# Optimization experiments

Measured on AMD Instinct MI355X. Metric: run time of the kernel, lower is better.

Reference implementation:

```python
import jax, jax.numpy as jnp
import numpy as np


def setup_inputs() -> dict:
    key = jax.random.key(0)
    ks = jax.random.split(key, 8)
    B, L, D = 4, 2048, 2048
    H, Dh, S = 24, 64, 64
    Di = H * Dh              # 1536
    P = H * (1 + 2 * S)      # 3096
    return {
        "hidden_states": jax.random.normal(ks[0], (B, L, D), jnp.float32),
        "norm_w": jnp.ones((D,), jnp.float32),
        "in_proj_w": jax.random.normal(ks[1], (2 * Di, D), jnp.float32) * 0.02,
        "in_proj_b": jnp.zeros((2 * Di,), jnp.float32),
        "conv_w": jax.random.normal(ks[2], (Di, 1, 4), jnp.float32) * 0.2,
        "conv_b": jnp.zeros((Di,), jnp.float32),
        "x_proj_w": jax.random.normal(ks[3], (P, Di), jnp.float32) * 0.02,
        "x_proj_b": jnp.zeros((P,), jnp.float32),
        "A_log": jnp.full((H,), np.log(0.5), jnp.float32),
        "log2_alpha_base": jnp.full((H,), -1.0, jnp.float32),
        "log2_beta": jnp.zeros((H,), jnp.float32),
        "surprise_ema": jnp.ones((H,), jnp.float32),
        "out_proj_w": jax.random.normal(ks[4], (D, Di), jnp.float32) * 0.02,
        "out_proj_b": jnp.zeros((D,), jnp.float32),
        "res_gate": jnp.full((1,), 1.0 / np.sqrt(2 * 24), jnp.float32),
    }


def reference(hidden_states, norm_w, in_proj_w, in_proj_b, conv_w, conv_b,
              x_proj_w, x_proj_b, A_log, log2_alpha_base, log2_beta,
              surprise_ema, out_proj_w, out_proj_b, res_gate):
    Bsz, L, D = hidden_states.shape
    H = A_log.shape[0]
    S = (x_proj_b.shape[0] // H - 1) // 2
    Di = in_proj_w.shape[0] // 2
    Dh = Di // H
    eps = jnp.finfo(jnp.float32).eps

    # RMSNorm
    x = hidden_states * jax.lax.rsqrt(jnp.mean(hidden_states ** 2, -1, keepdims=True) + eps) * norm_w
    # in_proj -> split x/z
    xz = x @ in_proj_w.T + in_proj_b
    x, z = xz[..., :Di], xz[..., Di:]
    # causal depthwise conv1d (kernel 4, left pad 3 == torch pad=3 then [:, :L])
    xc = jax.lax.conv_general_dilated(
        x.transpose(0, 2, 1), conv_w, (1,), [(3, 0)],
        dimension_numbers=("NCH", "OIH", "NCH"), feature_group_count=Di)
    x = jax.nn.silu((xc + conv_b[None, :, None]).transpose(0, 2, 1))
    # x_proj -> dt, B, C
    xp = (x @ x_proj_w.T + x_proj_b).reshape(Bsz, L, H, 1 + 2 * S)
    dt = xp[..., 0]
    Bs = xp[..., 1:1 + S]
    Cs = xp[..., 1 + S:]
    Bs = Bs / jnp.maximum(jnp.linalg.norm(Bs, axis=-1, keepdims=True), 1e-12)
    Cs = Cs / jnp.maximum(jnp.linalg.norm(Cs, axis=-1, keepdims=True), 1e-12)
    # dt-scaled log decay (dt_scale = softplus(dt))
    A = jnp.clip(A_log, -2.3, -0.01)[None, None, :] * jax.nn.softplus(dt)
    A_decay = jnp.exp(A)                       # [B, L, H]
    X = x.reshape(Bsz, L, H, Dh)

    # surprise-gate constants (eval mode: EMA buffer fixed)
    alpha_base = 1.0 - 2.0 ** jnp.clip(log2_alpha_base, -3.32, -0.015)   # [H]
    beta = 2.0 ** jnp.clip(log2_beta, -2.0, 2.0)                          # [H]

    def step(carry, xs):
        h, h_red = carry                      # [B,H,S,Dh], [B,H,S]
        x_t, a_t, B_t, C_t = xs               # [B,H,Dh], [B,H], [B,H,S], [B,H,S]
        u_red = B_t * x_t.mean(-1)[..., None]                 # mean over Dh of outer product
        diff = (1.0 - a_t)[..., None] * u_red                 # h_new_reduced - h_expected
        pe = jnp.mean(diff ** 2, -1)                          # [B,H]
        ns = pe / (surprise_ema[None, :] + 1e-6)
        boost = jax.nn.relu(jnp.tanh(beta[None, :] * ns))
        alpha = jnp.clip(alpha_base[None, :] + (1.0 - alpha_base[None, :]) * boost, 0.01, 0.999)
        u_t = B_t[..., None] * x_t[:, :, None, :]             # [B,H,S,Dh]
        h = alpha[..., None, None] * h + (1.0 - alpha)[..., None, None] * u_t
        h_red = h.mean(-1)
        y = jnp.einsum("bhs,bhsd->bhd", C_t, h)
        return (h, h_red), y

    h0 = jnp.zeros((Bsz, H, S, Dh), jnp.float32)
    hr0 = jnp.zeros((Bsz, H, S), jnp.float32)
    xs = (X.transpose(1, 0, 2, 3), A_decay.transpose(1, 0, 2),
          Bs.transpose(1, 0, 2, 3), Cs.transpose(1, 0, 2, 3))
    _, Yt = jax.lax.scan(step, (h0, hr0), xs)                 # [L,B,H,Dh]
    Y = Yt.transpose(1, 0, 2, 3).reshape(Bsz, L, Di)
    Y = Y * jax.nn.silu(z)
    out = Y @ out_proj_w.T + out_proj_b
    return hidden_states + res_gate * out
```

## Files before the change

### kernel.cpp

```cpp
#include <hip/hip_runtime.h>
#include <stdint.h>

#define BB 4
#define LLEN 2048
#define DMODEL 2048
#define NH 24
#define DH 64
#define SS 64
#define DI 1536
#define N2 3072
#define NP 3096
#define NP_PAD 3200
#define MROWS 8192
#define NCHUNK 16
#define QC 128
#define XP2LD 136

using bf16x8 = __bf16 __attribute__((ext_vector_type(8)));
using f32x4  = float __attribute__((ext_vector_type(4)));

__device__ __forceinline__ unsigned short f2bf(float f) {
  union { float f; unsigned int u; } v; v.f = f;
  unsigned int u = v.u + 0x7fffu + ((v.u >> 16) & 1u);
  return (unsigned short)(u >> 16);
}
__device__ __forceinline__ float bf2f(unsigned short h) {
  union { unsigned int u; float f; } v; v.u = ((unsigned int)h) << 16;
  return v.f;
}

__device__ __forceinline__ void gload16(const void* g, void* l) {
  __builtin_amdgcn_global_load_lds(
    reinterpret_cast<const __attribute__((address_space(1))) void*>(reinterpret_cast<uintptr_t>(g)),
    reinterpret_cast<__attribute__((address_space(3))) void*>((uint32_t)(reinterpret_cast<uintptr_t>(l))),
    16, 0, 0);
}

__global__ __launch_bounds__(256) void k_w2bf3(
    const float* __restrict__ s0, unsigned short* __restrict__ d0, int n0,
    const float* __restrict__ s1, unsigned short* __restrict__ d1, int n1s, int n1d,
    const float* __restrict__ s2, unsigned short* __restrict__ d2, int n2) {
  int i = blockIdx.x * 256 + threadIdx.x;
  if (i < n0) { d0[i] = f2bf(s0[i]); return; }
  i -= n0;
  if (i < n1d) { d1[i] = (i < n1s) ? f2bf(s1[i]) : (unsigned short)0; return; }
  i -= n1d;
  if (i < n2) d2[i] = f2bf(s2[i]);
}

__global__ __launch_bounds__(256) void k_rmsnorm(const float* __restrict__ hs,
                                                 const float* __restrict__ w,
                                                 unsigned short* __restrict__ out) {
  const int row = blockIdx.x;
  const int t = threadIdx.x;
  const float* x = hs + (size_t)row * DMODEL;
  float4 v0 = reinterpret_cast<const float4*>(x)[t * 2 + 0];
  float4 v1 = reinterpret_cast<const float4*>(x)[t * 2 + 1];
  float ss = v0.x * v0.x + v0.y * v0.y + v0.z * v0.z + v0.w * v0.w +
             v1.x * v1.x + v1.y * v1.y + v1.z * v1.z + v1.w * v1.w;
#pragma unroll
  for (int o = 32; o; o >>= 1) ss += __shfl_xor(ss, o);
  __shared__ float red[4];
  if ((t & 63) == 0) red[t >> 6] = ss;
  __syncthreads();
  ss = red[0] + red[1] + red[2] + red[3];
  const float r = rsqrtf(ss * (1.0f / DMODEL) + 1.1920928955078125e-07f);
  float4 w0 = reinterpret_cast<const float4*>(w)[t * 2 + 0];
  float4 w1 = reinterpret_cast<const float4*>(w)[t * 2 + 1];
  union { unsigned short u[8]; uint4 v; } pk;
  pk.u[0] = f2bf(v0.x * r * w0.x); pk.u[1] = f2bf(v0.y * r * w0.y);
  pk.u[2] = f2bf(v0.z * r * w0.z); pk.u[3] = f2bf(v0.w * r * w0.w);
  pk.u[4] = f2bf(v1.x * r * w1.x); pk.u[5] = f2bf(v1.y * r * w1.y);
  pk.u[6] = f2bf(v1.z * r * w1.z); pk.u[7] = f2bf(v1.w * r * w1.w);
  *reinterpret_cast<uint4*>(out + (size_t)row * DMODEL + t * 8) = pk.v;
}

template <int EPI>
__global__ __launch_bounds__(512, 2)
void k_gemm6(const unsigned short* __restrict__ A, const unsigned short* __restrict__ B,
             const float* __restrict__ bias, void* __restrict__ Cv,
             const float* __restrict__ resid, const float* __restrict__ gatep,
             int K, int NT_N, int Nout, int ldc) {
  constexpr int AELEM = 128 * 64;
  constexpr int BUFE = AELEM + 16384;
  __shared__ alignas(16) unsigned short sm[3 * BUFE];
  const int tid = threadIdx.x;
  const int lane = tid & 63, wid = tid >> 6;
  const int wm = wid >> 2, wn = wid & 3;
  const int fr = lane & 15, kg = lane >> 4;
  const int nwg = gridDim.x;
  const int wg = ((int)blockIdx.x & 7) * (nwg >> 3) + ((int)blockIdx.x >> 3);
  const int m0 = (wg / NT_N) * 128, n0 = (wg % NT_N) * 256;
  const int NT = K >> 6;

  const unsigned short* asrc[2];
  const unsigned short* bsrc[4];
#pragma unroll
  for (int li = 0; li < 2; ++li) {
    const int gi = li * 512 + tid, r = gi >> 3, q = gi & 7;
    asrc[li] = A + (size_t)(m0 + r) * K + ((q ^ (r & 7)) << 3);
  }
#pragma unroll
  for (int li = 0; li < 4; ++li) {
    const int gi = li * 512 + tid, r = gi >> 3, q = gi & 7;
    bsrc[li] = B + (size_t)(n0 + r) * K + ((q ^ (r & 7)) << 3);
  }
  const int wlds = wid * 64;

#define STG6(buf, ko)                                                          \
  { unsigned short* da_ = sm + (buf) * BUFE;                                   \
    gload16(asrc[0] + (ko), da_ + ((0 * 512 + wlds) << 3));                    \
    gload16(asrc[1] + (ko), da_ + ((1 * 512 + wlds) << 3));                    \
    unsigned short* db_ = sm + (buf) * BUFE + AELEM;                           \
    _Pragma("unroll") for (int li = 0; li < 4; ++li)                           \
      gload16(bsrc[li] + (ko), db_ + ((li * 512 + wlds) << 3)); }

#define ARD6(bufp, f, kk)                                                      \
  (*(const bf16x8*)((bufp) + (wm * 64 + (f) * 16 + fr) * 64 +                  \
      ((((kk) * 4 + kg) ^ (fr & 7)) << 3)))
#define BRD6(bufp, nf, kk)                                                     \
  (*(const bf16x8*)((bufp) + AELEM + (wn * 64 + (nf) * 16 + fr) * 64 +         \
      ((((kk) * 4 + kg) ^ (fr & 7)) << 3)))

  f32x4 acc[4][4] = {};

  STG6(0, 0)
  STG6(1, 64)
  asm volatile("s_waitcnt vmcnt(6)" ::: "memory");
  __builtin_amdgcn_s_barrier();

  int bc_i = 0;
  for (int t = 0; t < NT; ++t) {
    unsigned short* bc = sm + bc_i * BUFE;
    const int bn_i = (bc_i + 2 >= 3) ? (bc_i - 1) : (bc_i + 2);
    const bool st = (t + 2) < NT;
    if (st) STG6(bn_i, (t + 2) << 6)

    bf16x8 bfv[4][2], af[4][2];
#pragma unroll
    for (int nf = 0; nf < 4; ++nf) {
      bfv[nf][0] = BRD6(bc, nf, 0);
      bfv[nf][1] = BRD6(bc, nf, 1);
    }
#pragma unroll
    for (int mf = 0; mf < 4; ++mf) {
      af[mf][0] = ARD6(bc, mf, 0);
      af[mf][1] = ARD6(bc, mf, 1);
    }
    __builtin_amdgcn_sched_barrier(0);
    asm volatile("s_waitcnt lgkmcnt(0)" ::: "memory");
    __builtin_amdgcn_sched_barrier(0);
    __builtin_amdgcn_s_setprio(1);
#pragma unroll
    for (int mf = 0; mf < 4; ++mf)
#pragma unroll
      for (int nf = 0; nf < 4; ++nf)
#pragma unroll
        for (int kk = 0; kk < 2; ++kk)
          acc[mf][nf] = __builtin_amdgcn_mfma_f32_16x16x32_bf16(
              af[mf][kk], bfv[nf][kk], acc[mf][nf], 0, 0, 0);
    __builtin_amdgcn_s_setprio(0);

    if (st) { asm volatile("s_waitcnt vmcnt(6)" ::: "memory"); }
    else    { asm volatile("s_waitcnt vmcnt(0)" ::: "memory"); }
    __builtin_amdgcn_s_barrier();
    bc_i = (bc_i + 1 >= 3) ? 0 : (bc_i + 1);
  }

  float* Cf = (float*)Cv;
  unsigned short* Ch = (unsigned short*)Cv;
  const float rg = (EPI == 2) ? gatep[0] : 0.f;
#pragma unroll
  for (int nf = 0; nf < 4; ++nf) {
    const int col = n0 + wn * 64 + nf * 16 + fr;
    if (col >= Nout) continue;
    const float bv = bias[col];
    int h = 0, ep = 0;
    if (EPI == 3) {
      h = col / 129;
      const int e = col - h * 129;
      ep = (e == 0) ? 128 : (e - 1);
    }
#pragma unroll
    for (int mf = 0; mf < 4; ++mf) {
      const int rowb = m0 + wm * 64 + mf * 16 + kg * 4;
#pragma unroll
      for (int r = 0; r < 4; ++r) {
        const int row = rowb + r;
        float v = acc[mf][nf][r] + bv;
        if (EPI == 3) {
          const size_t dst =
              (((size_t)((row >> 11) * NH + h) << 11) + (row & (LLEN - 1))) * XP2LD + ep;
          Ch[dst] = f2bf(v);
        } else {
          const size_t o = (size_t)row * ldc + col;
          if (EPI == 1) {
            Ch[o] = f2bf(v);
          } else {
            v = resid[o] + rg * v;
            Cf[o] = v;
          }
        }
      }
    }
  }
#undef STG6
#undef ARD6
#undef BRD6
}

__global__ __launch_bounds__(256) void k_dwconv(const unsigned short* __restrict__ xz,
                                                const float* __restrict__ cw,
                                                const float* __restrict__ cb,
                                                unsigned short* __restrict__ out) {
  const int idx = blockIdx.x * 256 + threadIdx.x;
  const int c0 = (idx % 192) * 8;
  const int bl0 = (idx / 192) * 4;
  const int lpos0 = bl0 & (LLEN - 1);
  float w[8][4];
#pragma unroll
  for (int j = 0; j < 8; ++j) {
    const float4 wv = *(const float4*)(cw + (c0 + j) * 4);
    w[j][0] = wv.x; w[j][1] = wv.y; w[j][2] = wv.z; w[j][3] = wv.w;
  }
  float xr[7][8];
#pragma unroll
  for (int m = 0; m < 7; ++m) {
    uint4 xv = make_uint4(0u, 0u, 0u, 0u);
    if (lpos0 - 3 + m >= 0)
      xv = *(const uint4*)(xz + (size_t)(bl0 - 3 + m) * N2 + c0);
    const unsigned short* xs = (const unsigned short*)&xv;
#pragma unroll
    for (int j = 0; j < 8; ++j) xr[m][j] = bf2f(xs[j]);
  }
  const float4 cb0 = *(const float4*)(cb + c0);
  const float4 cb1 = *(const float4*)(cb + c0 + 4);
  const float cbv[8] = {cb0.x, cb0.y, cb0.z, cb0.w, cb1.x, cb1.y, cb1.z, cb1.w};
#pragma unroll
  for (int t4 = 0; t4 < 4; ++t4) {
    union { unsigned short u[8]; uint4 v; } pk;
#pragma unroll
    for (int j = 0; j < 8; ++j) {
      float a = cbv[j];
#pragma unroll
      for (int k = 0; k < 4; ++k) a = fmaf(w[j][k], xr[t4 + k][j], a);
      a = a / (1.f + __expf(-a));
      pk.u[j] = f2bf(a);
    }
    *(uint4*)(out + (size_t)(bl0 + t4) * DI + c0) = pk.v;
  }
}

__global__ __launch_bounds__(256) void k_prep2(const unsigned short* __restrict__ xp2,
                                               const unsigned short* __restrict__ xc,
                                               const float* __restrict__ A_log,
                                               const float* __restrict__ l2ab,
                                               const float* __restrict__ l2b,
                                               const float* __restrict__ se,
                                               float* __restrict__ al) {
  const int blk = blockIdx.x;
  const int w = threadIdx.x >> 6, lane = threadIdx.x & 63;
  const int bl = blk / 6, hq = blk % 6;
  const int h = hq * 4 + w;
  const float xv = bf2f(xc[(size_t)bl * DI + h * DH + lane]);
  float sx = xv;
#pragma unroll
  for (int o = 32; o; o >>= 1) sx += __shfl_xor(sx, o);
  if (lane == 0) {
    const int b = bl >> 11, l = bl & (LLEN - 1);
    const size_t r2 = ((size_t)(b * NH + h) << 11) + l;
    const float xmean = sx * (1.f / 64.f);
    const float dt = bf2f(xp2[r2 * XP2LD + 128]);
    const float sp = (dt > 20.f) ? dt : log1pf(expf(dt));
    const float Ac = fminf(fmaxf(A_log[h], -2.3f), -0.01f);
    const float aa = expf(Ac * sp);
    const float one_a = 1.f - aa;
    const float pe = one_a * one_a * xmean * xmean * (1.f / 64.f);
    const float ns = pe / (se[h] + 1e-6f);
    const float beta = exp2f(fminf(fmaxf(l2b[h], -2.f), 2.f));
    const float boost = fmaxf(tanhf(beta * ns), 0.f);
    const float ab = 1.f - exp2f(fminf(fmaxf(l2ab[h], -3.32f), -0.015f));
    al[r2] = fminf(fmaxf(ab + (1.f - ab) * boost, 0.01f), 0.999f);
  }
}

__global__ __launch_bounds__(256) void k_chunk1(
    const unsigned short* __restrict__ xp2, const unsigned short* __restrict__ xcg,
    const float* __restrict__ al, unsigned short* __restrict__ xz,
    unsigned short* __restrict__ Hbuf, float* __restrict__ Dc) {
  const int blk = blockIdx.x;
  const int bh = blk >> 4, c = blk & 15;
  const int b = bh / NH, h = bh % NH;
  const int tid = threadIdx.x, w = tid >> 6, lane = tid & 63;
  const int fr = lane & 15, kg = lane >> 4;
  const int rbase = b * LLEN + c * QC;
  const size_t rbase2 = ((size_t)bh << 11) + c * QC;

  __shared__ float lc[QC], ia[QC], escl[QC], rbA[QC], rcC[QC];
  __shared__ float wtot[2];
  __shared__ alignas(16) unsigned short XT[64][152];
  __shared__ alignas(16) unsigned short BsT[64][152];
  __shared__ alignas(16) unsigned short Pt[128][88];

  float a = 1.f, la = 0.f;
  if (tid < QC) { a = al[(size_t)bh * LLEN + c * QC + tid]; la = __logf(a); }
  float s = la;
#pragma unroll
  for (int o = 1; o < 64; o <<= 1) { float t2 = __shfl_up(s, o); if (lane >= o) s += t2; }
  if (tid < QC && lane == 63) wtot[w] = s;
  __syncthreads();
  if (tid < QC) { lc[tid] = s + ((w == 1) ? wtot[0] : 0.f); ia[tid] = 1.f - a; }
  __syncthreads();
  const float lcE = lc[QC - 1];
  if (tid < QC) escl[tid] = __expf(lcE - lc[tid]);
  if (tid == 0) Dc[blk] = __expf(lcE);
  __syncthreads();

  {
    const int r8 = tid >> 3, q8 = tid & 7;
#pragma unroll
    for (int it = 0; it < 4; ++it) {
      const int u = it * 32 + r8;
      const uint4 xv = *(const uint4*)(xcg + (size_t)(rbase + u) * DI + h * DH + q8 * 8);
      const unsigned short* xs = (const unsigned short*)&xv;
#pragma unroll
      for (int j = 0; j < 8; ++j) XT[q8 * 8 + j][u] = xs[j];
      const size_t prow = (rbase2 + u) * XP2LD;
      const uint4 bv = *(const uint4*)(xp2 + prow + q8 * 8);
      const uint4 cv = *(const uint4*)(xp2 + prow + 64 + q8 * 8);
      const unsigned short* bsv = (const unsigned short*)&bv;
      const unsigned short* csv = (const unsigned short*)&cv;
      float bb[8], sb = 0.f, sc2 = 0.f;
#pragma unroll
      for (int j = 0; j < 8; ++j) {
        bb[j] = bf2f(bsv[j]);
        sb = fmaf(bb[j], bb[j], sb);
        const float cc = bf2f(csv[j]);
        sc2 = fmaf(cc, cc, sc2);
      }
      sb += __shfl_xor(sb, 1); sb += __shfl_xor(sb, 2); sb += __shfl_xor(sb, 4);
      sc2 += __shfl_xor(sc2, 1); sc2 += __shfl_xor(sc2, 2); sc2 += __shfl_xor(sc2, 4);
      const float rcpB = 1.f / fmaxf(sqrtf(sb), 1e-12f);
      const float e = escl[u] * ia[u] * rcpB;
#pragma unroll
      for (int j = 0; j < 8; ++j) BsT[q8 * 8 + j][u] = f2bf(bb[j] * e);
      if (q8 == 0) {
        rbA[u] = ia[u] * rcpB;
        rcC[u] = 1.f / fmaxf(sqrtf(sc2), 1e-12f);
      }
    }
  }
  __syncthreads();

  bf16x8 cf[2][2];
#pragma unroll
  for (int fi = 0; fi < 2; ++fi)
#pragma unroll
    for (int kk = 0; kk < 2; ++kk) {
      const int t = w * 32 + fi * 16 + fr;
      const uint4 v = *(const uint4*)(xp2 + (rbase2 + t) * XP2LD + 64 + kk * 32 + kg * 8);
      cf[fi][kk] = *(const bf16x8*)&v;
    }

  float lct[2][4], rct[2][4];
#pragma unroll
  for (int fi = 0; fi < 2; ++fi)
#pragma unroll
    for (int r = 0; r < 4; ++r) {
      const int t = w * 32 + fi * 16 + kg * 4 + r;
      lct[fi][r] = lc[t];
      rct[fi][r] = rcC[t];
    }

  f32x4 yacc[2][4] = {};
  f32x4 hacc[4] = {};
#pragma unroll
  for (int ut = 0; ut < 2; ++ut) {
    f32x4 g[2][4] = {};
#pragma unroll
    for (int kk = 0; kk < 2; ++kk)
#pragma unroll
      for (int fj = 0; fj < 4; ++fj) {
        const int u = ut * 64 + fj * 16 + fr;
        const uint4 v = *(const uint4*)(xp2 + (rbase2 + u) * XP2LD + kk * 32 + kg * 8);
        const bf16x8 bfrag = *(const bf16x8*)&v;
#pragma unroll
        for (int fi = 0; fi < 2; ++fi)
          g[fi][fj] = __builtin_amdgcn_mfma_f32_16x16x32_bf16(cf[fi][kk], bfrag, g[fi][fj], 0, 0, 0);
      }
#pragma unroll
    for (int fi = 0; fi < 2; ++fi)
#pragma unroll
      for (int fj = 0; fj < 4; ++fj) {
        const int u = ut * 64 + fj * 16 + fr;
        const float lcu = lc[u], sbu = rbA[u];
#pragma unroll
        for (int r = 0; r < 4; ++r) {
          const int t = w * 32 + fi * 16 + kg * 4 + r;
          const float v = (t >= u) ? g[fi][fj][r] * __expf(lct[fi][r] - lcu) * sbu * rct[fi][r] : 0.f;
          Pt[t][fj * 16 + fr] = f2bf(v);
        }
      }
#pragma unroll
    for (int kk = 0; kk < 2; ++kk) {
      bf16x8 xf[4];
#pragma unroll
      for (int fj = 0; fj < 4; ++fj)
        xf[fj] = *(const bf16x8*)&XT[fj * 16 + fr][ut * 64 + kk * 32 + kg * 8];
      bf16x8 pf[2];
#pragma unroll
      for (int fi = 0; fi < 2; ++fi)
        pf[fi] = *(const bf16x8*)&Pt[w * 32 + fi * 16 + fr][kk * 32 + kg * 8];
#pragma unroll
      for (int fi = 0; fi < 2; ++fi)
#pragma unroll
        for (int fj = 0; fj < 4; ++fj)
          yacc[fi][fj] = __builtin_amdgcn_mfma_f32_16x16x32_bf16(pf[fi], xf[fj], yacc[fi][fj], 0, 0, 0);
      const bf16x8 xh = *(const bf16x8*)&XT[w * 16 + fr][ut * 64 + kk * 32 + kg * 8];
#pragma unroll
      for (int fi = 0; fi < 4; ++fi) {
        const bf16x8 bs = *(const bf16x8*)&BsT[fi * 16 + fr][ut * 64 + kk * 32 + kg * 8];
        hacc[fi] = __builtin_amdgcn_mfma_f32_16x16x32_bf16(bs, xh, hacc[fi], 0, 0, 0);
      }
    }
  }
#pragma unroll
  for (int fi = 0; fi < 2; ++fi)
#pragma unroll
    for (int fj = 0; fj < 4; ++fj)
#pragma unroll
      for (int r = 0; r < 4; ++r) {
        const int t = w * 32 + fi * 16 + kg * 4 + r;
        const int d = fj * 16 + fr;
        xz[(size_t)(rbase + t) * N2 + h * DH + d] = f2bf(yacc[fi][fj][r]);
      }
  const int dcol = w * 16 + fr;
#pragma unroll
  for (int fi = 0; fi < 4; ++fi) {
    ushort4 pk;
    pk.x = f2bf(hacc[fi][0]); pk.y = f2bf(hacc[fi][1]);
    pk.z = f2bf(hacc[fi][2]); pk.w = f2bf(hacc[fi][3]);
    *(ushort4*)(Hbuf + ((size_t)blk * 64 + dcol) * 64 + fi * 16 + kg * 4) = pk;
  }
}

__global__ __launch_bounds__(256) void k_carry(unsigned short* __restrict__ Hbuf,
                                               const float* __restrict__ Dc) {
  const int bh = blockIdx.x, tid = threadIdx.x;
  float carry[16];
#pragma unroll
  for (int j = 0; j < 16; ++j) carry[j] = 0.f;
  for (int c = 0; c < NCHUNK; ++c) {
    unsigned short* p = Hbuf + (((size_t)(bh * NCHUNK + c)) << 12) + tid * 16;
    const uint4 v0 = *(const uint4*)(p);
    const uint4 v1 = *(const uint4*)(p + 8);
    const unsigned short* hs0 = (const unsigned short*)&v0;
    const unsigned short* hs1 = (const unsigned short*)&v1;
    float hl[16];
#pragma unroll
    for (int j = 0; j < 8; ++j) { hl[j] = bf2f(hs0[j]); hl[8 + j] = bf2f(hs1[j]); }
    uint4 o0, o1;
    unsigned short* os0 = (unsigned short*)&o0;
    unsigned short* os1 = (unsigned short*)&o1;
#pragma unroll
    for (int j = 0; j < 8; ++j) { os0[j] = f2bf(carry[j]); os1[j] = f2bf(carry[8 + j]); }
    *(uint4*)(p) = o0;
    *(uint4*)(p + 8) = o1;
    const float dc = Dc[bh * NCHUNK + c];
#pragma unroll
    for (int j = 0; j < 16; ++j) carry[j] = fmaf(dc, carry[j], hl[j]);
  }
}

__global__ __launch_bounds__(256) void k_chunk2(
    const unsigned short* __restrict__ xp2, const float* __restrict__ al,
    const unsigned short* __restrict__ Hbuf, const unsigned short* __restrict__ xz,
    unsigned short* __restrict__ xcg) {
  const int blk = blockIdx.x;
  const int bh = blk >> 4, c = blk & 15;
  const int b = bh / NH, h = bh % NH;
  const int tid = threadIdx.x, w = tid >> 6, lane = tid & 63;
  const int fr = lane & 15, kg = lane >> 4;
  const int rbase = b * LLEN + c * QC;
  const size_t rbase2 = ((size_t)bh << 11) + c * QC;
  __shared__ float lc[QC], rc2[QC];
  __shared__ float wtot[2];
  float a = 1.f, la = 0.f;
  if (tid < QC) { a = al[(size_t)bh * LLEN + c * QC + tid]; la = __logf(a); }
  float s = la;
#pragma unroll
  for (int o = 1; o < 64; o <<= 1) { float t2 = __shfl_up(s, o); if (lane >= o) s += t2; }
  if (tid < QC && lane == 63) wtot[w] = s;
  __syncthreads();
  if (tid < QC) lc[tid] = s + ((w == 1) ? wtot[0] : 0.f);
  __syncthreads();
  bf16x8 cf[2][2];
#pragma unroll
  for (int fi = 0; fi < 2; ++fi) {
    const int t = w * 32 + fi * 16 + fr;
    float ss = 0.f;
#pragma unroll
    for (int kk = 0; kk < 2; ++kk) {
      const uint4 v = *(const uint4*)(xp2 + (rbase2 + t) * XP2LD + 64 + kk * 32 + kg * 8);
      cf[fi][kk] = *(const bf16x8*)&v;
      const unsigned short* cs = (const unsigned short*)&v;
#pragma unroll
      for (int q = 0; q < 8; ++q) { const float cc = bf2f(cs[q]); ss = fmaf(cc, cc, ss); }
    }
    ss += __shfl_xor(ss, 16);
    ss += __shfl_xor(ss, 32);
    if (kg == 0) rc2[t] = 1.f / fmaxf(sqrtf(ss), 1e-12f);
  }
  bf16x8 hf[4][2];
#pragma unroll
  for (int fj = 0; fj < 4; ++fj)
#pragma unroll
    for (int kk = 0; kk < 2; ++kk) {
      const uint4 v = *(const uint4*)(Hbuf + ((size_t)blk * 64 + fj * 16 + fr) * 64 + kk * 32 + kg * 8);
      hf[fj][kk] = *(const bf16x8*)&v;
    }
  __syncthreads();
  f32x4 y[2][4] = {};
#pragma unroll
  for (int kk = 0; kk < 2; ++kk)
#pragma unroll
    for (int fi = 0; fi < 2; ++fi)
#pragma unroll
      for (int fj = 0; fj < 4; ++fj)
        y[fi][fj] = __builtin_amdgcn_mfma_f32_16x16x32_bf16(cf[fi][kk], hf[fj][kk], y[fi][fj], 0, 0, 0);
#pragma unroll
  for (int fi = 0; fi < 2; ++fi)
#pragma unroll
    for (int fj = 0; fj < 4; ++fj)
#pragma unroll
      for (int r = 0; r < 4; ++r) {
        const int t = w * 32 + fi * 16 + kg * 4 + r;
        const int d = fj * 16 + fr;
        const float scl = rc2[t] * __expf(lc[t]);
        const size_t rowg = (size_t)(rbase + t);
        const float yv = y[fi][fj][r] * scl + bf2f(xz[rowg * N2 + h * DH + d]);
        const float zv = bf2f(xz[rowg * N2 + DI + h * DH + d]);
        const float g = yv * (zv / (1.f + __expf(-zv)));
        xcg[rowg * DI + h * DH + d] = f2bf(g);
      }
}

extern "C" void kernel_launch(void* const* d_in, const int* in_sizes, int n_in,
                              void* d_out, int out_size, void* d_ws, size_t ws_size,
                              hipStream_t stream) {
  const float* hs     = (const float*)d_in[0];
  const float* norm_w = (const float*)d_in[1];
  const float* in_w   = (const float*)d_in[2];
  const float* in_b   = (const float*)d_in[3];
  const float* cw     = (const float*)d_in[4];
  const float* cb     = (const float*)d_in[5];
  const float* xw     = (const float*)d_in[6];
  const float* xb     = (const float*)d_in[7];
  const float* A_log  = (const float*)d_in[8];
  const float* l2ab   = (const float*)d_in[9];
  const float* l2b    = (const float*)d_in[10];
  const float* se     = (const float*)d_in[11];
  const float* ow     = (const float*)d_in[12];
  const float* ob     = (const float*)d_in[13];
  const float* rg     = (const float*)d_in[14];
  float* out = (float*)d_out;

  char* ws = (char*)d_ws;
  unsigned short* xnorm = (unsigned short*)(ws);
  unsigned short* wA    = (unsigned short*)(ws + 33554432ull);
  unsigned short* wX    = (unsigned short*)(ws + 46137344ull);
  unsigned short* wO    = (unsigned short*)(ws + 55967744ull);
  unsigned short* xz    = (unsigned short*)(ws + 62259200ull);
  unsigned short* xp2   = (unsigned short*)(ws + 112590848ull);
  unsigned short* xcg   = xnorm;
  unsigned short* Hbuf  = wA;
  float* al             = (float*)(ws + 46137344ull);
  float* Dc             = (float*)(ws + 46137344ull + 786432ull);

  k_w2bf3<<<56064, 256, 0, stream>>>(in_w, wA, N2 * DMODEL,
                                     xw, wX, NP * DI, NP_PAD * DI,
                                     ow, wO, DMODEL * DI);

  k_rmsnorm<<<MROWS, 256, 0, stream>>>(hs, norm_w, xnorm);
  k_gemm6<1><<<768, 512, 0, stream>>>(xnorm, wA, in_b, xz, nullptr, nullptr,
                                      DMODEL, 12, N2, N2);
  k_dwconv<<<(MROWS / 4) * 192 / 256, 256, 0, stream>>>(xz, cw, cb, xcg);
  k_gemm6<3><<<832, 512, 0, stream>>>(xcg, wX, xb, xp2, nullptr, nullptr,
                                      DI, 13, NP, 0);
  k_prep2<<<MROWS * 6, 256, 0, stream>>>(xp2, xcg, A_log, l2ab, l2b, se, al);

  k_chunk1<<<BB * NH * NCHUNK, 256, 0, stream>>>(xp2, xcg, al, xz, Hbuf, Dc);
  k_carry<<<BB * NH, 256, 0, stream>>>(Hbuf, Dc);
  k_chunk2<<<BB * NH * NCHUNK, 256, 0, stream>>>(xp2, al, Hbuf, xz, xcg);

  k_gemm6<2><<<512, 512, 0, stream>>>(xcg, wO, ob, out, hs, rg,
                                      DI, 8, DMODEL, DMODEL);
}
```

Measured before the change: 507.7 us.

## Fuse alpha gating into x_proj epilogue and merge weight conversion with RMSNorm

Removes the separate k_prep2 kernel. The per-head x mean is now computed inside the depthwise conv kernel with shuffles, and the dt softplus/alpha computation runs in the x_proj GEMM epilogue, using per-head constants precomputed in a new merged pre-kernel. The weight bf16 conversion, RMSNorm and head constants now share a single launch, and the xp2 row stride shrinks to 128 because dt is no longer stored. This saves two launches and one pass over xc/xp2, at the cost of transcendental work inside the GEMM epilogue and new workspace buffers.

Result: faster. 485.7 us (-4.3%).

```diff
diff --git a/kernel.cpp b/kernel.cpp
--- a/kernel.cpp
+++ b/kernel.cpp
@@ -14,7 +14,8 @@
 #define MROWS 8192
 #define NCHUNK 16
 #define QC 128
-#define XP2LD 136
+#define XP2LD 128
+#define WBLK 56064
 
 using bf16x8 = __bf16 __attribute__((ext_vector_type(8)));
 using f32x4  = float __attribute__((ext_vector_type(4)));
@@ -36,23 +37,36 @@
     16, 0, 0);
 }
 
-__global__ __launch_bounds__(256) void k_w2bf3(
-    const float* __restrict__ s0, unsigned short* __restrict__ d0, int n0,
-    const float* __restrict__ s1, unsigned short* __restrict__ d1, int n1s, int n1d,
-    const float* __restrict__ s2, unsigned short* __restrict__ d2, int n2) {
-  int i = blockIdx.x * 256 + threadIdx.x;
-  if (i < n0) { d0[i] = f2bf(s0[i]); return; }
-  i -= n0;
-  if (i < n1d) { d1[i] = (i < n1s) ? f2bf(s1[i]) : (unsigned short)0; return; }
-  i -= n1d;
-  if (i < n2) d2[i] = f2bf(s2[i]);
-}
-
-__global__ __launch_bounds__(256) void k_rmsnorm(const float* __restrict__ hs,
-                                                 const float* __restrict__ w,
-                                                 unsigned short* __restrict__ out) {
-  const int row = blockIdx.x;
+__global__ __launch_bounds__(256) void k_pre(
+    const float* __restrict__ in_w, unsigned short* __restrict__ wA,
+    const float* __restrict__ xw, unsigned short* __restrict__ wX,
+    const float* __restrict__ ow, unsigned short* __restrict__ wO,
+    const float* __restrict__ hs, const float* __restrict__ norm_w,
+    unsigned short* __restrict__ xnorm,
+    const float* __restrict__ A_log, const float* __restrict__ l2ab,
+    const float* __restrict__ l2b, const float* __restrict__ se,
+    float* __restrict__ hc) {
+  const int blk = blockIdx.x;
   const int t = threadIdx.x;
+  if (blk < WBLK) {
+    int i = blk * 256 + t;
+    if (i < N2 * DMODEL) { wA[i] = f2bf(in_w[i]); return; }
+    i -= N2 * DMODEL;
+    if (i < NP_PAD * DI) { wX[i] = (i < NP * DI) ? f2bf(xw[i]) : (unsigned short)0; return; }
+    i -= NP_PAD * DI;
+    wO[i] = f2bf(ow[i]);
+    return;
+  }
+  if (blk == WBLK + MROWS) {
+    if (t < NH) {
+      hc[t]          = fminf(fmaxf(A_log[t], -2.3f), -0.01f);
+      hc[NH + t]     = exp2f(fminf(fmaxf(l2b[t], -2.f), 2.f));
+      hc[2 * NH + t] = 1.f - exp2f(fminf(fmaxf(l2ab[t], -3.32f), -0.015f));
+      hc[3 * NH + t] = 1.f / (se[t] + 1e-6f);
+    }
+    return;
+  }
+  const int row = blk - WBLK;
   const float* x = hs + (size_t)row * DMODEL;
   float4 v0 = reinterpret_cast<const float4*>(x)[t * 2 + 0];
   float4 v1 = reinterpret_cast<const float4*>(x)[t * 2 + 1];
@@ -65,14 +79,14 @@
   __syncthreads();
   ss = red[0] + red[1] + red[2] + red[3];
   const float r = rsqrtf(ss * (1.0f / DMODEL) + 1.1920928955078125e-07f);
-  float4 w0 = reinterpret_cast<const float4*>(w)[t * 2 + 0];
-  float4 w1 = reinterpret_cast<const float4*>(w)[t * 2 + 1];
+  float4 w0 = reinterpret_cast<const float4*>(norm_w)[t * 2 + 0];
+  float4 w1 = reinterpret_cast<const float4*>(norm_w)[t * 2 + 1];
   union { unsigned short u[8]; uint4 v; } pk;
   pk.u[0] = f2bf(v0.x * r * w0.x); pk.u[1] = f2bf(v0.y * r * w0.y);
   pk.u[2] = f2bf(v0.z * r * w0.z); pk.u[3] = f2bf(v0.w * r * w0.w);
   pk.u[4] = f2bf(v1.x * r * w1.x); pk.u[5] = f2bf(v1.y * r * w1.y);
   pk.u[6] = f2bf(v1.z * r * w1.z); pk.u[7] = f2bf(v1.w * r * w1.w);
-  *reinterpret_cast<uint4*>(out + (size_t)row * DMODEL + t * 8) = pk.v;
+  *reinterpret_cast<uint4*>(xnorm + (size_t)row * DMODEL + t * 8) = pk.v;
 }
 
 template <int EPI>
@@ -80,6 +94,8 @@
 void k_gemm6(const unsigned short* __restrict__ A, const unsigned short* __restrict__ B,
              const float* __restrict__ bias, void* __restrict__ Cv,
              const float* __restrict__ resid, const float* __restrict__ gatep,
+             const float* __restrict__ xmean, float* __restrict__ al,
+             const float* __restrict__ hc,
              int K, int NT_N, int Nout, int ldc) {
   constexpr int AELEM = 128 * 64;
   constexpr int BUFE = AELEM + 16384;
@@ -175,25 +191,49 @@
     const int col = n0 + wn * 64 + nf * 16 + fr;
     if (col >= Nout) continue;
     const float bv = bias[col];
-    int h = 0, ep = 0;
     if (EPI == 3) {
-      h = col / 129;
+      const int h = col / 129;
       const int e = col - h * 129;
-      ep = (e == 0) ? 128 : (e - 1);
-    }
-#pragma unroll
-    for (int mf = 0; mf < 4; ++mf) {
-      const int rowb = m0 + wm * 64 + mf * 16 + kg * 4;
-#pragma unroll
-      for (int r = 0; r < 4; ++r) {
-        const int row = rowb + r;
-        float v = acc[mf][nf][r] + bv;
-        if (EPI == 3) {
-          const size_t dst =
-              (((size_t)((row >> 11) * NH + h) << 11) + (row & (LLEN - 1))) * XP2LD + ep;
-          Ch[dst] = f2bf(v);
-        } else {
-          const size_t o = (size_t)row * ldc + col;
+      if (e == 0) {
+        const float Ac = hc[h], bet = hc[NH + h], ab = hc[2 * NH + h], rse = hc[3 * NH + h];
+#pragma unroll
+        for (int mf = 0; mf < 4; ++mf) {
+          const int rowb = m0 + wm * 64 + mf * 16 + kg * 4;
+#pragma unroll
+          for (int r = 0; r < 4; ++r) {
+            const int row = rowb + r;
+            const float dt = acc[mf][nf][r] + bv;
+            const float sp = (dt > 20.f) ? dt : log1pf(expf(dt));
+            const float one_a = 1.f - expf(Ac * sp);
+            const size_t r2 = (((size_t)((row >> 11) * NH + h)) << 11) + (row & (LLEN - 1));
+            const float xm = xmean[r2];
+            const float pe = one_a * one_a * xm * xm * (1.f / 64.f);
+            const float boost = fmaxf(tanhf(bet * pe * rse), 0.f);
+            al[r2] = fminf(fmaxf(ab + (1.f - ab) * boost, 0.01f), 0.999f);
+          }
+        }
+      } else {
+        const int ep = e - 1;
+#pragma unroll
+        for (int mf = 0; mf < 4; ++mf) {
+          const int rowb = m0 + wm * 64 + mf * 16 + kg * 4;
+#pragma unroll
+          for (int r = 0; r < 4; ++r) {
+            const int row = rowb + r;
+            const size_t dst =
+                (((size_t)((row >> 11) * NH + h) << 11) + (row & (LLEN - 1))) * XP2LD + ep;
+            Ch[dst] = f2bf(acc[mf][nf][r] + bv);
+          }
+        }
+      }
+    } else {
+#pragma unroll
+      for (int mf = 0; mf < 4; ++mf) {
+        const int rowb = m0 + wm * 64 + mf * 16 + kg * 4;
+#pragma unroll
+        for (int r = 0; r < 4; ++r) {
+          const size_t o = (size_t)(rowb + r) * ldc + col;
+          float v = acc[mf][nf][r] + bv;
           if (EPI == 1) {
             Ch[o] = f2bf(v);
           } else {
@@ -212,7 +252,8 @@
 __global__ __launch_bounds__(256) void k_dwconv(const unsigned short* __restrict__ xz,
                                                 const float* __restrict__ cw,
                                                 const float* __restrict__ cb,
-                                                unsigned short* __restrict__ out) {
+                                                unsigned short* __restrict__ out,
+                                                float* __restrict__ xmean) {
   const int idx = blockIdx.x * 256 + threadIdx.x;
   const int c0 = (idx % 192) * 8;
   const int bl0 = (idx / 192) * 4;
@@ -236,6 +277,7 @@
   const float4 cb0 = *(const float4*)(cb + c0);
   const float4 cb1 = *(const float4*)(cb + c0 + 4);
   const float cbv[8] = {cb0.x, cb0.y, cb0.z, cb0.w, cb1.x, cb1.y, cb1.z, cb1.w};
+  float hsum[4] = {0.f, 0.f, 0.f, 0.f};
 #pragma unroll
   for (int t4 = 0; t4 < 4; ++t4) {
     union { unsigned short u[8]; uint4 v; } pk;
@@ -245,42 +287,22 @@
 #pragma unroll
       for (int k = 0; k < 4; ++k) a = fmaf(w[j][k], xr[t4 + k][j], a);
       a = a / (1.f + __expf(-a));
+      hsum[t4] += a;
       pk.u[j] = f2bf(a);
     }
     *(uint4*)(out + (size_t)(bl0 + t4) * DI + c0) = pk.v;
   }
-}
-
-__global__ __launch_bounds__(256) void k_prep2(const unsigned short* __restrict__ xp2,
-                                               const unsigned short* __restrict__ xc,
-                                               const float* __restrict__ A_log,
-                                               const float* __restrict__ l2ab,
-                                               const float* __restrict__ l2b,
-                                               const float* __restrict__ se,
-                                               float* __restrict__ al) {
-  const int blk = blockIdx.x;
-  const int w = threadIdx.x >> 6, lane = threadIdx.x & 63;
-  const int bl = blk / 6, hq = blk % 6;
-  const int h = hq * 4 + w;
-  const float xv = bf2f(xc[(size_t)bl * DI + h * DH + lane]);
-  float sx = xv;
-#pragma unroll
-  for (int o = 32; o; o >>= 1) sx += __shfl_xor(sx, o);
-  if (lane == 0) {
-    const int b = bl >> 11, l = bl & (LLEN - 1);
-    const size_t r2 = ((size_t)(b * NH + h) << 11) + l;
-    const float xmean = sx * (1.f / 64.f);
-    const float dt = bf2f(xp2[r2 * XP2LD + 128]);
-    const float sp = (dt > 20.f) ? dt : log1pf(expf(dt));
-    const float Ac = fminf(fmaxf(A_log[h], -2.3f), -0.01f);
-    const float aa = expf(Ac * sp);
-    const float one_a = 1.f - aa;
-    const float pe = one_a * one_a * xmean * xmean * (1.f / 64.f);
-    const float ns = pe / (se[h] + 1e-6f);
-    const float beta = exp2f(fminf(fmaxf(l2b[h], -2.f), 2.f));
-    const float boost = fmaxf(tanhf(beta * ns), 0.f);
-    const float ab = 1.f - exp2f(fminf(fmaxf(l2ab[h], -3.32f), -0.015f));
-    al[r2] = fminf(fmaxf(ab + (1.f - ab) * boost, 0.01f), 0.999f);
+#pragma unroll
+  for (int o = 1; o < 8; o <<= 1) {
+#pragma unroll
+    for (int t4 = 0; t4 < 4; ++t4) hsum[t4] += __shfl_xor(hsum[t4], o);
+  }
+  if ((threadIdx.x & 7) == 0) {
+    const int h = (idx % 192) >> 3;
+    const int b = bl0 >> 11;
+    float4 xm = make_float4(hsum[0] * (1.f / 64.f), hsum[1] * (1.f / 64.f),
+                            hsum[2] * (1.f / 64.f), hsum[3] * (1.f / 64.f));
+    *(float4*)(xmean + (((size_t)(b * NH + h)) << 11) + lpos0) = xm;
   }
 }
 
@@ -572,27 +594,27 @@
   unsigned short* wO    = (unsigned short*)(ws + 55967744ull);
   unsigned short* xz    = (unsigned short*)(ws + 62259200ull);
   unsigned short* xp2   = (unsigned short*)(ws + 112590848ull);
+  float* xmean          = (float*)(ws + 162922496ull);
+  float* al             = (float*)(ws + 163708928ull);
+  float* Dc             = (float*)(ws + 164495360ull);
+  float* hc             = (float*)(ws + 164501504ull);
   unsigned short* xcg   = xnorm;
   unsigned short* Hbuf  = wA;
-  float* al             = (float*)(ws + 46137344ull);
-  float* Dc             = (float*)(ws + 46137344ull + 786432ull);
-
-  k_w2bf3<<<56064, 256, 0, stream>>>(in_w, wA, N2 * DMODEL,
-                                     xw, wX, NP * DI, NP_PAD * DI,
-                                     ow, wO, DMODEL * DI);
-
-  k_rmsnorm<<<MROWS, 256, 0, stream>>>(hs, norm_w, xnorm);
+
+  k_pre<<<WBLK + MROWS + 1, 256, 0, stream>>>(in_w, wA, xw, wX, ow, wO,
+                                              hs, norm_w, xnorm,
+                                              A_log, l2ab, l2b, se, hc);
   k_gemm6<1><<<768, 512, 0, stream>>>(xnorm, wA, in_b, xz, nullptr, nullptr,
+                                      nullptr, nullptr, nullptr,
                                       DMODEL, 12, N2, N2);
-  k_dwconv<<<(MROWS / 4) * 192 / 256, 256, 0, stream>>>(xz, cw, cb, xcg);
+  k_dwconv<<<(MROWS / 4) * 192 / 256, 256, 0, stream>>>(xz, cw, cb, xcg, xmean);
   k_gemm6<3><<<832, 512, 0, stream>>>(xcg, wX, xb, xp2, nullptr, nullptr,
+                                      xmean, al, hc,
                                       DI, 13, NP, 0);
-  k_prep2<<<MROWS * 6, 256, 0, stream>>>(xp2, xcg, A_log, l2ab, l2b, se, al);
-
   k_chunk1<<<BB * NH * NCHUNK, 256, 0, stream>>>(xp2, xcg, al, xz, Hbuf, Dc);
   k_carry<<<BB * NH, 256, 0, stream>>>(Hbuf, Dc);
   k_chunk2<<<BB * NH * NCHUNK, 256, 0, stream>>>(xp2, al, Hbuf, xz, xcg);
-
   k_gemm6<2><<<512, 512, 0, stream>>>(xcg, wO, ob, out, hs, rg,
+                                      nullptr, nullptr, nullptr,
                                       DI, 8, DMODEL, DMODEL);
 }
```
